# Optimization experiments

Hardware: AMD Instinct MI355X
Metric: run time of the kernel (lower is better)

Reference implementation:

```python
import jax, jax.numpy as jnp
import numpy as np

N_NODES = 100000
N_EDGES = 1600000
D_IN = 128
HIDDEN = 128
N_CLASS = 10
N_LAYERS = 3


def setup_inputs() -> dict:
    key = jax.random.key(0)
    ks = jax.random.split(key, 12)
    x = jax.random.normal(ks[0], (N_NODES, D_IN), dtype=jnp.float32)
    edge_index = jax.random.randint(ks[1], (2, N_EDGES), 0, N_NODES, dtype=jnp.int64)
    edge_weight = jax.random.uniform(ks[2], (N_EDGES,), dtype=jnp.float32)
    # Per-layer GIN MLP params. D_IN == HIDDEN so all 3 layers stack cleanly.
    s = 1.0 / np.sqrt(HIDDEN)
    Wa = jax.random.uniform(ks[3], (N_LAYERS, HIDDEN, HIDDEN), minval=-s, maxval=s, dtype=jnp.float32)
    ba = jax.random.uniform(ks[4], (N_LAYERS, HIDDEN), minval=-s, maxval=s, dtype=jnp.float32)
    Wb = jax.random.uniform(ks[5], (N_LAYERS, HIDDEN, HIDDEN), minval=-s, maxval=s, dtype=jnp.float32)
    bb = jax.random.uniform(ks[6], (N_LAYERS, HIDDEN), minval=-s, maxval=s, dtype=jnp.float32)
    fcW = jax.random.uniform(ks[7], (HIDDEN, N_CLASS), minval=-s, maxval=s, dtype=jnp.float32)
    fcb = jax.random.uniform(ks[8], (N_CLASS,), minval=-s, maxval=s, dtype=jnp.float32)
    return {"x": x, "edge_index": edge_index, "edge_weight": edge_weight,
            "Wa": Wa, "ba": ba, "Wb": Wb, "bb": bb, "fcW": fcW, "fcb": fcb}


def reference(x, edge_index, edge_weight, Wa, ba, Wb, bb, fcW, fcb):
    # NOTE: edge_weight is loaded in the original forward but never used
    # (GINConv is invoked with only (x, edge_index)); we faithfully ignore it.
    src = edge_index[0]
    dst = edge_index[1]
    h = x
    for i in range(N_LAYERS):
        # GIN aggregation: (1 + eps) * h + sum_{j in N(i)} h_j, with eps = 0
        agg = jax.ops.segment_sum(h[src], dst, num_segments=N_NODES)  # [N, H]
        z = h + agg
        # 2-layer MLP: Linear -> ELU -> Linear -> ELU
        z = jax.nn.elu(z @ Wa[i] + ba[i])
        h = jax.nn.elu(z @ Wb[i] + bb[i])
    return h @ fcW + fcb  # [N, n_class]
```

## Files before the change

kernel.cpp:

```cpp
#include <hip/hip_runtime.h>
#include <hip/hip_bf16.h>
#include <math.h>

#define N_NODES 100000
#define N_PAD 100032
#define N_EDGES 1600000
#define HID 128
#define N_CLASS 10

#define NR2 256
#define RANGE2 391
#define PCAP2 8192
#define P_BLOCKS 512
#define P_SLICE (N_EDGES / P_BLOCKS)

typedef float f32x4 __attribute__((ext_vector_type(4)));
typedef short short8 __attribute__((ext_vector_type(8)));
typedef unsigned short us4 __attribute__((ext_vector_type(4)));

__device__ __forceinline__ unsigned short f2bf(float x) {
    unsigned u = __float_as_uint(x);
    unsigned r = u + 0x7FFF + ((u >> 16) & 1);
    return (unsigned short)(r >> 16);
}
__device__ __forceinline__ float bf2f(unsigned short h) {
    return __uint_as_float(((unsigned)h) << 16);
}
__device__ __forceinline__ float elu(float x) {
    return x > 0.f ? x : (expf(x) - 1.f);
}


__global__ __launch_bounds__(256) void part_k(const int* __restrict__ src,
                                              const int* __restrict__ dst,
                                              int* __restrict__ gcnt,
                                              unsigned* __restrict__ gbuf) {
    __shared__ unsigned stash[P_SLICE];
    __shared__ unsigned char rbuf[P_SLICE];
    __shared__ int hist[NR2], cur[NR2], base[NR2];
    hist[threadIdx.x] = 0;
    cur[threadIdx.x] = 0;
    __syncthreads();
    const int e0 = blockIdx.x * P_SLICE;
    for (int i = threadIdx.x; i < P_SLICE; i += 256) {
        unsigned s = (unsigned)src[e0 + i];
        unsigned d = (unsigned)dst[e0 + i];
        unsigned r = d / RANGE2;
        unsigned dloc = d - r * RANGE2;
        stash[i] = s | (dloc << 17);
        rbuf[i] = (unsigned char)r;
        atomicAdd(&hist[r], 1);
    }
    __syncthreads();
    base[threadIdx.x] = atomicAdd(&gcnt[threadIdx.x], hist[threadIdx.x]);
    __syncthreads();
    for (int i = threadIdx.x; i < P_SLICE; i += 256) {
        unsigned r = rbuf[i];
        int off = atomicAdd(&cur[r], 1);
        int pos = base[r] + off;
        if (pos < PCAP2) gbuf[(size_t)r * PCAP2 + pos] = stash[i];
    }
}

__global__ void scanc_k(const int* __restrict__ gcnt, int* __restrict__ colbase,
                        int* __restrict__ row_ptr) {
    __shared__ int sh[NR2];
    int v = gcnt[threadIdx.x];
    sh[threadIdx.x] = v;
    __syncthreads();
    for (int off = 1; off < NR2; off <<= 1) {
        int t = (threadIdx.x >= off) ? sh[threadIdx.x - off] : 0;
        __syncthreads();
        sh[threadIdx.x] += t;
        __syncthreads();
    }
    colbase[threadIdx.x] = sh[threadIdx.x] - v;
    if (threadIdx.x == 0) row_ptr[N_NODES] = N_EDGES;
}

__global__ __launch_bounds__(256) void csort_k(const unsigned* __restrict__ gbuf,
                                               const int* __restrict__ gcnt,
                                               const int* __restrict__ colbase,
                                               int* __restrict__ row_ptr,
                                               int* __restrict__ col) {
    __shared__ int sorted[PCAP2];
    __shared__ int hist[512];
    __shared__ int cnt[512];
    __shared__ int run[400];
    const int q = blockIdx.x;
    const int tid = threadIdx.x;
    const int n2 = gcnt[q];
    const int cb = colbase[q];
    const int node0 = q * RANGE2;
    const unsigned* buf = gbuf + (size_t)q * PCAP2;

    hist[tid] = 0; hist[tid + 256] = 0;
    __syncthreads();
    for (int i = tid; i < n2; i += 256)
        atomicAdd(&hist[buf[i] >> 17], 1);
    __syncthreads();
    cnt[tid] = hist[tid];
    cnt[tid + 256] = hist[tid + 256];
    __syncthreads();
    for (int off = 1; off < 512; off <<= 1) {
        int v0 = (tid >= off) ? hist[tid - off] : 0;
        int v1 = hist[tid + 256 - off];
        __syncthreads();
        hist[tid] += v0;
        hist[tid + 256] += v1;
        __syncthreads();
    }
#pragma unroll
    for (int b = 0; b < 2; b++) {
        int i = tid + 256 * b;
        if (i < RANGE2) {
            int excl = hist[i] - cnt[i];
            run[i] = excl;
            int node = node0 + i;
            if (node < N_NODES) row_ptr[node] = cb + excl;
        }
    }
    __syncthreads();
    for (int i = tid; i < n2; i += 256) {
        unsigned w = buf[i];
        int pos = atomicAdd(&run[w >> 17], 1);
        sorted[pos] = (int)(w & 0x1FFFF);
    }
    __syncthreads();
    for (int i = tid; i < n2; i += 256) col[cb + i] = sorted[i];
}

__global__ __launch_bounds__(256) void cast_k(const float* __restrict__ x,
                                              unsigned short* __restrict__ hb) {
    int i = blockIdx.x * blockDim.x + threadIdx.x;
    if (i < N_NODES * (HID / 4)) {
        float4 v = ((const float4*)x)[i];
        us4 o = {f2bf(v.x), f2bf(v.y), f2bf(v.z), f2bf(v.w)};
        ((us4*)hb)[i] = o;
    }
}

__global__ void wsplit_k(const float* __restrict__ Wa, const float* __restrict__ Wb,
                         unsigned short* __restrict__ Whp,
                         unsigned short* __restrict__ Wlp) {
    int f = blockIdx.x * blockDim.x + threadIdx.x;
    if (f >= 6 * 16384) return;
    int g = f >> 14;
    int r = f & 16383;
    int j = r & 7;
    int L = (r >> 3) & 63;
    int t = r >> 9;
    int kb = t >> 3, nt = t & 7;
    int k = kb * 32 + ((L >> 4) & 3) * 8 + j;
    int n = nt * 16 + (L & 15);
    int layer = g >> 1;
    const float* W = (g & 1) ? Wb : Wa;
    float w = W[layer * 16384 + k * 128 + n];
    unsigned short hi = f2bf(w);
    unsigned short lo = f2bf(w - bf2f(hi));
    Whp[f] = hi;
    Wlp[f] = lo;
}

__global__ void fcsplit_k(const float* __restrict__ fcW,
                          unsigned short* __restrict__ fcWph,
                          unsigned short* __restrict__ fcWpl) {
    int f = blockIdx.x * blockDim.x + threadIdx.x;
    if (f >= 2048) return;
    int j = f & 7;
    int L = (f >> 3) & 63;
    int kb = f >> 9;
    int k = kb * 32 + ((L >> 4) & 3) * 8 + j;
    int n = L & 15;
    float w = (n < N_CLASS) ? fcW[k * N_CLASS + n] : 0.f;
    unsigned short hi = f2bf(w);
    unsigned short lo = f2bf(w - bf2f(hi));
    fcWph[f] = hi;
    fcWpl[f] = lo;
}

__device__ __forceinline__ float4 us4f(us4 v) {
    float4 o;
    o.x = bf2f(v.x); o.y = bf2f(v.y); o.z = bf2f(v.z); o.w = bf2f(v.w);
    return o;
}

__global__ __launch_bounds__(256) void agg_k(const unsigned short* __restrict__ h,
                                             const int* __restrict__ row_ptr,
                                             const int* __restrict__ col,
                                             float* __restrict__ z) {
    const int half = (blockIdx.x * blockDim.x + threadIdx.x) >> 5;
    const int lane = threadIdx.x & 31;
    const int halfbase = threadIdx.x & 32;
    if (half >= N_NODES) return;
    const us4* hp = (const us4*)h;
    float4 acc = us4f(hp[(size_t)half * 32 + lane]);
    const int beg = row_ptr[half];
    const int end = row_ptr[half + 1];

    for (int base = beg; base < end; base += 32) {
        const int n = min(32, end - base);
        int myidx = (lane < n) ? col[base + lane] : 0;
        int j = 0;
        for (; j + 4 <= n; j += 4) {
            int i0 = __shfl(myidx, halfbase + j + 0, 64);
            int i1 = __shfl(myidx, halfbase + j + 1, 64);
            int i2 = __shfl(myidx, halfbase + j + 2, 64);
            int i3 = __shfl(myidx, halfbase + j + 3, 64);
            float4 v0 = us4f(hp[(size_t)i0 * 32 + lane]);
            float4 v1 = us4f(hp[(size_t)i1 * 32 + lane]);
            float4 v2 = us4f(hp[(size_t)i2 * 32 + lane]);
            float4 v3 = us4f(hp[(size_t)i3 * 32 + lane]);
            acc.x += v0.x; acc.y += v0.y; acc.z += v0.z; acc.w += v0.w;
            acc.x += v1.x; acc.y += v1.y; acc.z += v1.z; acc.w += v1.w;
            acc.x += v2.x; acc.y += v2.y; acc.z += v2.z; acc.w += v2.w;
            acc.x += v3.x; acc.y += v3.y; acc.z += v3.z; acc.w += v3.w;
        }
        for (; j < n; j++) {
            int i0 = __shfl(myidx, halfbase + j, 64);
            float4 v0 = us4f(hp[(size_t)i0 * 32 + lane]);
            acc.x += v0.x; acc.y += v0.y; acc.z += v0.z; acc.w += v0.w;
        }
    }
    ((float4*)z)[(size_t)half * 32 + lane] = acc;
}

__device__ __forceinline__ void gemm_phase(
    const unsigned short* Aph_, const unsigned short* Apl_,
    const unsigned short* __restrict__ Whi_g,
    const unsigned short* __restrict__ Wlo_g,
    const float* __restrict__ bias, int tid, f32x4 acc[2][4]) {
    const int L = tid & 63;
    const int w = tid >> 6;
    const int mt0 = (w >> 1) * 2;
    const int nt0 = (w & 1) * 4;
    const int lan15 = L & 15;
#pragma unroll
    for (int n = 0; n < 4; n++) {
        float b = bias[(nt0 + n) * 16 + lan15];
        f32x4 bv = {b, b, b, b};
        acc[0][n] = bv;
        acc[1][n] = bv;
    }
#pragma unroll
    for (int kb = 0; kb < 4; kb++) {
        short8 ah0 = *(const short8*)&Aph_[(((mt0 + 0) * 4 + kb) * 64 + L) * 8];
        short8 ah1 = *(const short8*)&Aph_[(((mt0 + 1) * 4 + kb) * 64 + L) * 8];
        short8 al0 = *(const short8*)&Apl_[(((mt0 + 0) * 4 + kb) * 64 + L) * 8];
        short8 al1 = *(const short8*)&Apl_[(((mt0 + 1) * 4 + kb) * 64 + L) * 8];
#pragma unroll
        for (int n = 0; n < 4; n++) {
            int widx = ((kb * 8 + nt0 + n) * 64 + L) * 8;
            short8 bh = *(const short8*)&Whi_g[widx];
            short8 bl = *(const short8*)&Wlo_g[widx];
            acc[0][n] = __builtin_amdgcn_mfma_f32_16x16x32_bf16(ah0, bh, acc[0][n], 0, 0, 0);
            acc[1][n] = __builtin_amdgcn_mfma_f32_16x16x32_bf16(ah1, bh, acc[1][n], 0, 0, 0);
            acc[0][n] = __builtin_amdgcn_mfma_f32_16x16x32_bf16(al0, bh, acc[0][n], 0, 0, 0);
            acc[1][n] = __builtin_amdgcn_mfma_f32_16x16x32_bf16(al1, bh, acc[1][n], 0, 0, 0);
            acc[0][n] = __builtin_amdgcn_mfma_f32_16x16x32_bf16(ah0, bl, acc[0][n], 0, 0, 0);
            acc[1][n] = __builtin_amdgcn_mfma_f32_16x16x32_bf16(ah1, bl, acc[1][n], 0, 0, 0);
        }
    }
}

template <int FC>
__device__ __forceinline__ void mlp_body(
    const float* __restrict__ zin,
    const unsigned short* __restrict__ Wahp, const unsigned short* __restrict__ Walp,
    const unsigned short* __restrict__ Wbhp, const unsigned short* __restrict__ Wblp,
    const float* __restrict__ ba, const float* __restrict__ bb,
    unsigned short* __restrict__ hout,
    const unsigned short* __restrict__ fcWph, const unsigned short* __restrict__ fcWpl,
    const float* __restrict__ fcb, float* __restrict__ out) {
    __shared__ unsigned short Aph[8192];
    __shared__ unsigned short Apl[8192];

    const int tid = threadIdx.x;
    const int L = tid & 63;
    const int w = tid >> 6;
    const int mt0 = (w >> 1) * 2;
    const int nt0 = (w & 1) * 4;
    const int lan15 = L & 15;
    const int quad = L >> 4;
    const size_t node_base = (size_t)blockIdx.x * 64;

    {
        const float4* zin4 = (const float4*)(zin + node_base * HID);
#pragma unroll
        for (int r = 0; r < 8; r++) {
            int f = tid + 256 * r;
            int m = f >> 5;
            int k0 = (f & 31) * 4;
            float4 zv = zin4[f];
            int kb = k0 >> 5;
            int q = (k0 & 31) >> 3;
            int j0 = k0 & 7;
            int idx = (((m >> 4) * 4 + kb) * 64 + ((m & 15) + 16 * q)) * 8 + j0;
            unsigned short hx = f2bf(zv.x), hy = f2bf(zv.y),
                           hz = f2bf(zv.z), hw = f2bf(zv.w);
            us4 h4 = {hx, hy, hz, hw};
            us4 l4 = {f2bf(zv.x - bf2f(hx)), f2bf(zv.y - bf2f(hy)),
                      f2bf(zv.z - bf2f(hz)), f2bf(zv.w - bf2f(hw))};
            *(us4*)&Aph[idx] = h4;
            *(us4*)&Apl[idx] = l4;
        }
    }
    __syncthreads();

    {
        f32x4 acc[2][4];
        gemm_phase(Aph, Apl, Wahp, Walp, ba, tid, acc);
        __syncthreads();
#pragma unroll
        for (int i = 0; i < 2; i++) {
#pragma unroll
            for (int n = 0; n < 4; n++) {
                int kdim = (nt0 + n) * 16 + lan15;
                int kb2 = kdim >> 5;
                int q2 = (kdim & 31) >> 3;
                int j2 = kdim & 7;
#pragma unroll
                for (int r = 0; r < 4; r++) {
                    float v = elu(acc[i][n][r]);
                    int mrow = quad * 4 + r;
                    unsigned short hi = f2bf(v);
                    unsigned short lo = f2bf(v - bf2f(hi));
                    int idx = (((mt0 + i) * 4 + kb2) * 64 + (mrow + 16 * q2)) * 8 + j2;
                    Aph[idx] = hi;
                    Apl[idx] = lo;
                }
            }
        }
    }
    __syncthreads();

    {
        f32x4 acc[2][4];
        gemm_phase(Aph, Apl, Wbhp, Wblp, bb, tid, acc);
        if (FC == 0) {
#pragma unroll
            for (int i = 0; i < 2; i++) {
#pragma unroll
                for (int n = 0; n < 4; n++) {
                    int ncol = (nt0 + n) * 16 + lan15;
#pragma unroll
                    for (int r = 0; r < 4; r++) {
                        int mrow = (mt0 + i) * 16 + quad * 4 + r;
                        hout[(node_base + mrow) * HID + ncol] = f2bf(elu(acc[i][n][r]));
                    }
                }
            }
        } else {
            __syncthreads();
#pragma unroll
            for (int i = 0; i < 2; i++) {
#pragma unroll
                for (int n = 0; n < 4; n++) {
                    int kdim = (nt0 + n) * 16 + lan15;
                    int kb2 = kdim >> 5;
                    int q2 = (kdim & 31) >> 3;
                    int j2 = kdim & 7;
#pragma unroll
                    for (int r = 0; r < 4; r++) {
                        float v = elu(acc[i][n][r]);
                        int mrow = quad * 4 + r;
                        int idx = (((mt0 + i) * 4 + kb2) * 64 + (mrow + 16 * q2)) * 8 + j2;
                        Aph[idx] = f2bf(v);
                    }
                }
            }
            __syncthreads();
            if ((w & 1) == 0) {
#pragma unroll
                for (int i = 0; i < 2; i++) {
                    int mt = mt0 + i;
                    float b = (lan15 < N_CLASS) ? fcb[lan15] : 0.f;
                    f32x4 acc2 = {b, b, b, b};
#pragma unroll
                    for (int kb = 0; kb < 4; kb++) {
                        short8 a = *(const short8*)&Aph[((mt * 4 + kb) * 64 + L) * 8];
                        short8 bh = *(const short8*)&fcWph[(kb * 64 + L) * 8];
                        short8 bl = *(const short8*)&fcWpl[(kb * 64 + L) * 8];
                        acc2 = __builtin_amdgcn_mfma_f32_16x16x32_bf16(a, bh, acc2, 0, 0, 0);
                        acc2 = __builtin_amdgcn_mfma_f32_16x16x32_bf16(a, bl, acc2, 0, 0, 0);
                    }
#pragma unroll
                    for (int r = 0; r < 4; r++) {
                        size_t node = node_base + mt * 16 + quad * 4 + r;
                        if (node < N_NODES && lan15 < N_CLASS)
                            out[node * N_CLASS + lan15] = acc2[r];
                    }
                }
            }
        }
    }
}

__global__ __launch_bounds__(256) void mlp2_k(
    const float* __restrict__ zin,
    const unsigned short* __restrict__ Wahp, const unsigned short* __restrict__ Walp,
    const unsigned short* __restrict__ Wbhp, const unsigned short* __restrict__ Wblp,
    const float* __restrict__ ba, const float* __restrict__ bb,
    unsigned short* __restrict__ hout) {
    mlp_body<0>(zin, Wahp, Walp, Wbhp, Wblp, ba, bb, hout,
                nullptr, nullptr, nullptr, nullptr);
}

__global__ __launch_bounds__(256) void mlp3_k(
    const float* __restrict__ zin,
    const unsigned short* __restrict__ Wahp, const unsigned short* __restrict__ Walp,
    const unsigned short* __restrict__ Wbhp, const unsigned short* __restrict__ Wblp,
    const float* __restrict__ ba, const float* __restrict__ bb,
    const unsigned short* __restrict__ fcWph, const unsigned short* __restrict__ fcWpl,
    const float* __restrict__ fcb, float* __restrict__ out) {
    mlp_body<1>(zin, Wahp, Walp, Wbhp, Wblp, ba, bb, nullptr,
                fcWph, fcWpl, fcb, out);
}


extern "C" void kernel_launch(void* const* d_in, const int* in_sizes, int n_in,
                              void* d_out, int out_size, void* d_ws, size_t ws_size,
                              hipStream_t stream) {
    const float* x = (const float*)d_in[0];
    const int* ei = (const int*)d_in[1];
    const float* Wa = (const float*)d_in[3];
    const float* ba = (const float*)d_in[4];
    const float* Wb = (const float*)d_in[5];
    const float* bb = (const float*)d_in[6];
    const float* fcW = (const float*)d_in[7];
    const float* fcb = (const float*)d_in[8];
    float* out = (float*)d_out;

    const int* src = ei;
    const int* dst = ei + N_EDGES;

    char* w = (char*)d_ws;
    float* zbuf = (float*)w;          w += (size_t)N_PAD * HID * 4;
    unsigned short* hb = (unsigned short*)w; w += (size_t)N_PAD * HID * 2;
    int* row_ptr = (int*)w;  w += ((size_t)N_NODES + 8) * 4;
    int* gcnt = (int*)w;     w += NR2 * 4;
    int* colbase = (int*)w;  w += NR2 * 4;
    int* col = (int*)w;      w += (size_t)N_EDGES * 4;
    unsigned short* Whp = (unsigned short*)w; w += 6 * 16384 * 2;
    unsigned short* Wlp = (unsigned short*)w; w += 6 * 16384 * 2;
    unsigned short* fcWph = (unsigned short*)w; w += 2048 * 2;
    unsigned short* fcWpl = (unsigned short*)w; w += 2048 * 2;
    unsigned* gbuf = (unsigned*)w; w += (size_t)NR2 * PCAP2 * 4;

    wsplit_k<<<(6 * 16384 + 255) / 256, 256, 0, stream>>>(Wa, Wb, Whp, Wlp);
    fcsplit_k<<<8, 256, 0, stream>>>(fcW, fcWph, fcWpl);
    cast_k<<<(N_NODES * (HID / 4) + 255) / 256, 256, 0, stream>>>(x, hb);

    hipMemsetAsync(gcnt, 0, NR2 * 4, stream);
    part_k<<<P_BLOCKS, 256, 0, stream>>>(src, dst, gcnt, gbuf);
    scanc_k<<<1, 256, 0, stream>>>(gcnt, colbase, row_ptr);
    csort_k<<<NR2, 256, 0, stream>>>(gbuf, gcnt, colbase, row_ptr, col);

    const int AGG_BLOCKS = (N_NODES * 32 + 255) / 256;
    const int MLP_BLOCKS = (N_NODES + 63) / 64;

    agg_k<<<AGG_BLOCKS, 256, 0, stream>>>(hb, row_ptr, col, zbuf);
    mlp2_k<<<MLP_BLOCKS, 256, 0, stream>>>(zbuf, Whp, Wlp, Whp + 16384, Wlp + 16384,
                                           ba, bb, hb);
    agg_k<<<AGG_BLOCKS, 256, 0, stream>>>(hb, row_ptr, col, zbuf);
    mlp2_k<<<MLP_BLOCKS, 256, 0, stream>>>(zbuf, Whp + 2 * 16384, Wlp + 2 * 16384,
                                           Whp + 3 * 16384, Wlp + 3 * 16384,
                                           ba + 128, bb + 128, hb);
    agg_k<<<AGG_BLOCKS, 256, 0, stream>>>(hb, row_ptr, col, zbuf);
    mlp3_k<<<MLP_BLOCKS, 256, 0, stream>>>(zbuf, Whp + 4 * 16384, Wlp + 4 * 16384,
                                           Whp + 5 * 16384, Wlp + 5 * 16384,
                                           ba + 256, bb + 256,
                                           fcWph, fcWpl, fcb, out);
}
```

Measured before the change: 455.2 us.

## Fuse neighbor aggregation into MLP layer kernels with ping-pong bf16 buffers

Folds the gather-sum aggregation into the per-layer MLP kernel: each 64-node block has its half-waves aggregate 8 nodes each and write the split hi/lo bf16 tiles straight into shared memory. This removes the fp32 z buffer round trip through HBM and three kernel launches per forward. Two bf16 h buffers now alternate between layers so that reads and writes do not overlap. The cost is that the irregular gather now shares a block with the MFMA work and its register and LDS budget, and each block processes its 8 nodes per half-wave serially, which may reduce latency hiding for the gathers.

```diff
diff --git a/kernel.cpp b/kernel.cpp
--- a/kernel.cpp
+++ b/kernel.cpp
@@ -28,6 +28,11 @@
 }
 __device__ __forceinline__ float elu(float x) {
     return x > 0.f ? x : (expf(x) - 1.f);
+}
+__device__ __forceinline__ float4 us4f(us4 v) {
+    float4 o;
+    o.x = bf2f(v.x); o.y = bf2f(v.y); o.z = bf2f(v.z); o.w = bf2f(v.w);
+    return o;
 }
 
 
@@ -179,52 +184,6 @@
     fcWpl[f] = lo;
 }
 
-__device__ __forceinline__ float4 us4f(us4 v) {
-    float4 o;
-    o.x = bf2f(v.x); o.y = bf2f(v.y); o.z = bf2f(v.z); o.w = bf2f(v.w);
-    return o;
-}
-
-__global__ __launch_bounds__(256) void agg_k(const unsigned short* __restrict__ h,
-                                             const int* __restrict__ row_ptr,
-                                             const int* __restrict__ col,
-                                             float* __restrict__ z) {
-    const int half = (blockIdx.x * blockDim.x + threadIdx.x) >> 5;
-    const int lane = threadIdx.x & 31;
-    const int halfbase = threadIdx.x & 32;
-    if (half >= N_NODES) return;
-    const us4* hp = (const us4*)h;
-    float4 acc = us4f(hp[(size_t)half * 32 + lane]);
-    const int beg = row_ptr[half];
-    const int end = row_ptr[half + 1];
-
-    for (int base = beg; base < end; base += 32) {
-        const int n = min(32, end - base);
-        int myidx = (lane < n) ? col[base + lane] : 0;
-        int j = 0;
-        for (; j + 4 <= n; j += 4) {
-            int i0 = __shfl(myidx, halfbase + j + 0, 64);
-            int i1 = __shfl(myidx, halfbase + j + 1, 64);
-            int i2 = __shfl(myidx, halfbase + j + 2, 64);
-            int i3 = __shfl(myidx, halfbase + j + 3, 64);
-            float4 v0 = us4f(hp[(size_t)i0 * 32 + lane]);
-            float4 v1 = us4f(hp[(size_t)i1 * 32 + lane]);
-            float4 v2 = us4f(hp[(size_t)i2 * 32 + lane]);
-            float4 v3 = us4f(hp[(size_t)i3 * 32 + lane]);
-            acc.x += v0.x; acc.y += v0.y; acc.z += v0.z; acc.w += v0.w;
-            acc.x += v1.x; acc.y += v1.y; acc.z += v1.z; acc.w += v1.w;
-            acc.x += v2.x; acc.y += v2.y; acc.z += v2.z; acc.w += v2.w;
-            acc.x += v3.x; acc.y += v3.y; acc.z += v3.z; acc.w += v3.w;
-        }
-        for (; j < n; j++) {
-            int i0 = __shfl(myidx, halfbase + j, 64);
-            float4 v0 = us4f(hp[(size_t)i0 * 32 + lane]);
-            acc.x += v0.x; acc.y += v0.y; acc.z += v0.z; acc.w += v0.w;
-        }
-    }
-    ((float4*)z)[(size_t)half * 32 + lane] = acc;
-}
-
 __device__ __forceinline__ void gemm_phase(
     const unsigned short* Aph_, const unsigned short* Apl_,
     const unsigned short* __restrict__ Whi_g,
@@ -264,8 +223,9 @@
 }
 
 template <int FC>
-__device__ __forceinline__ void mlp_body(
-    const float* __restrict__ zin,
+__device__ __forceinline__ void layer_body(
+    const unsigned short* __restrict__ hin,
+    const int* __restrict__ row_ptr, const int* __restrict__ col,
     const unsigned short* __restrict__ Wahp, const unsigned short* __restrict__ Walp,
     const unsigned short* __restrict__ Wbhp, const unsigned short* __restrict__ Wblp,
     const float* __restrict__ ba, const float* __restrict__ bb,
@@ -285,22 +245,54 @@
     const size_t node_base = (size_t)blockIdx.x * 64;
 
     {
-        const float4* zin4 = (const float4*)(zin + node_base * HID);
-#pragma unroll
-        for (int r = 0; r < 8; r++) {
-            int f = tid + 256 * r;
-            int m = f >> 5;
-            int k0 = (f & 31) * 4;
-            float4 zv = zin4[f];
-            int kb = k0 >> 5;
-            int q = (k0 & 31) >> 3;
-            int j0 = k0 & 7;
-            int idx = (((m >> 4) * 4 + kb) * 64 + ((m & 15) + 16 * q)) * 8 + j0;
-            unsigned short hx = f2bf(zv.x), hy = f2bf(zv.y),
-                           hz = f2bf(zv.z), hw = f2bf(zv.w);
-            us4 h4 = {hx, hy, hz, hw};
-            us4 l4 = {f2bf(zv.x - bf2f(hx)), f2bf(zv.y - bf2f(hy)),
-                      f2bf(zv.z - bf2f(hz)), f2bf(zv.w - bf2f(hw))};
+        const int hwv = tid >> 5;
+        const int lane = tid & 31;
+        const int halfbase = tid & 32;
+        const us4* hp = (const us4*)hin;
+        const int k0 = lane * 4;
+        const int kb = k0 >> 5;
+        const int q = (k0 & 31) >> 3;
+        const int j0 = k0 & 7;
+#pragma unroll 1
+        for (int i = 0; i < 8; i++) {
+            const int m = hwv * 8 + i;
+            const int node = (int)node_base + m;
+            float4 acc = {0.f, 0.f, 0.f, 0.f};
+            if (node < N_NODES) {
+                acc = us4f(hp[(size_t)node * 32 + lane]);
+                const int beg = row_ptr[node];
+                const int end = row_ptr[node + 1];
+                for (int base = beg; base < end; base += 32) {
+                    const int n = min(32, end - base);
+                    int myidx = (lane < n) ? col[base + lane] : 0;
+                    int j = 0;
+                    for (; j + 4 <= n; j += 4) {
+                        int i0 = __shfl(myidx, halfbase + j + 0, 64);
+                        int i1 = __shfl(myidx, halfbase + j + 1, 64);
+                        int i2 = __shfl(myidx, halfbase + j + 2, 64);
+                        int i3 = __shfl(myidx, halfbase + j + 3, 64);
+                        float4 v0 = us4f(hp[(size_t)i0 * 32 + lane]);
+                        float4 v1 = us4f(hp[(size_t)i1 * 32 + lane]);
+                        float4 v2 = us4f(hp[(size_t)i2 * 32 + lane]);
+                        float4 v3 = us4f(hp[(size_t)i3 * 32 + lane]);
+                        acc.x += v0.x; acc.y += v0.y; acc.z += v0.z; acc.w += v0.w;
+                        acc.x += v1.x; acc.y += v1.y; acc.z += v1.z; acc.w += v1.w;
+                        acc.x += v2.x; acc.y += v2.y; acc.z += v2.z; acc.w += v2.w;
+                        acc.x += v3.x; acc.y += v3.y; acc.z += v3.z; acc.w += v3.w;
+                    }
+                    for (; j < n; j++) {
+                        int i0 = __shfl(myidx, halfbase + j, 64);
+                        float4 v0 = us4f(hp[(size_t)i0 * 32 + lane]);
+                        acc.x += v0.x; acc.y += v0.y; acc.z += v0.z; acc.w += v0.w;
+                    }
+                }
+            }
+            const int idx = (((m >> 4) * 4 + kb) * 64 + ((m & 15) + 16 * q)) * 8 + j0;
+            unsigned short sx = f2bf(acc.x), sy = f2bf(acc.y),
+                           sz = f2bf(acc.z), sw = f2bf(acc.w);
+            us4 h4 = {sx, sy, sz, sw};
+            us4 l4 = {f2bf(acc.x - bf2f(sx)), f2bf(acc.y - bf2f(sy)),
+                      f2bf(acc.z - bf2f(sz)), f2bf(acc.w - bf2f(sw))};
             *(us4*)&Aph[idx] = h4;
             *(us4*)&Apl[idx] = l4;
         }
@@ -396,25 +388,27 @@
     }
 }
 
-__global__ __launch_bounds__(256) void mlp2_k(
-    const float* __restrict__ zin,
+__global__ __launch_bounds__(256) void layer_mid_k(
+    const unsigned short* __restrict__ hin,
+    const int* __restrict__ row_ptr, const int* __restrict__ col,
     const unsigned short* __restrict__ Wahp, const unsigned short* __restrict__ Walp,
     const unsigned short* __restrict__ Wbhp, const unsigned short* __restrict__ Wblp,
     const float* __restrict__ ba, const float* __restrict__ bb,
     unsigned short* __restrict__ hout) {
-    mlp_body<0>(zin, Wahp, Walp, Wbhp, Wblp, ba, bb, hout,
-                nullptr, nullptr, nullptr, nullptr);
-}
-
-__global__ __launch_bounds__(256) void mlp3_k(
-    const float* __restrict__ zin,
+    layer_body<0>(hin, row_ptr, col, Wahp, Walp, Wbhp, Wblp, ba, bb, hout,
+                  nullptr, nullptr, nullptr, nullptr);
+}
+
+__global__ __launch_bounds__(256) void layer_fc_k(
+    const unsigned short* __restrict__ hin,
+    const int* __restrict__ row_ptr, const int* __restrict__ col,
     const unsigned short* __restrict__ Wahp, const unsigned short* __restrict__ Walp,
     const unsigned short* __restrict__ Wbhp, const unsigned short* __restrict__ Wblp,
     const float* __restrict__ ba, const float* __restrict__ bb,
     const unsigned short* __restrict__ fcWph, const unsigned short* __restrict__ fcWpl,
     const float* __restrict__ fcb, float* __restrict__ out) {
-    mlp_body<1>(zin, Wahp, Walp, Wbhp, Wblp, ba, bb, nullptr,
-                fcWph, fcWpl, fcb, out);
+    layer_body<1>(hin, row_ptr, col, Wahp, Walp, Wbhp, Wblp, ba, bb, nullptr,
+                  fcWph, fcWpl, fcb, out);
 }
 
 
@@ -435,8 +429,8 @@
     const int* dst = ei + N_EDGES;
 
     char* w = (char*)d_ws;
-    float* zbuf = (float*)w;          w += (size_t)N_PAD * HID * 4;
-    unsigned short* hb = (unsigned short*)w; w += (size_t)N_PAD * HID * 2;
+    unsigned short* hbA = (unsigned short*)w; w += (size_t)N_PAD * HID * 2;
+    unsigned short* hbB = (unsigned short*)w; w += (size_t)N_PAD * HID * 2;
     int* row_ptr = (int*)w;  w += ((size_t)N_NODES + 8) * 4;
     int* gcnt = (int*)w;     w += NR2 * 4;
     int* colbase = (int*)w;  w += NR2 * 4;
@@ -449,26 +443,25 @@
 
     wsplit_k<<<(6 * 16384 + 255) / 256, 256, 0, stream>>>(Wa, Wb, Whp, Wlp);
     fcsplit_k<<<8, 256, 0, stream>>>(fcW, fcWph, fcWpl);
-    cast_k<<<(N_NODES * (HID / 4) + 255) / 256, 256, 0, stream>>>(x, hb);
+    cast_k<<<(N_NODES * (HID / 4) + 255) / 256, 256, 0, stream>>>(x, hbA);
 
     hipMemsetAsync(gcnt, 0, NR2 * 4, stream);
     part_k<<<P_BLOCKS, 256, 0, stream>>>(src, dst, gcnt, gbuf);
     scanc_k<<<1, 256, 0, stream>>>(gcnt, colbase, row_ptr);
     csort_k<<<NR2, 256, 0, stream>>>(gbuf, gcnt, colbase, row_ptr, col);
 
-    const int AGG_BLOCKS = (N_NODES * 32 + 255) / 256;
-    const int MLP_BLOCKS = (N_NODES + 63) / 64;
-
-    agg_k<<<AGG_BLOCKS, 256, 0, stream>>>(hb, row_ptr, col, zbuf);
-    mlp2_k<<<MLP_BLOCKS, 256, 0, stream>>>(zbuf, Whp, Wlp, Whp + 16384, Wlp + 16384,
-                                           ba, bb, hb);
-    agg_k<<<AGG_BLOCKS, 256, 0, stream>>>(hb, row_ptr, col, zbuf);
-    mlp2_k<<<MLP_BLOCKS, 256, 0, stream>>>(zbuf, Whp + 2 * 16384, Wlp + 2 * 16384,
-                                           Whp + 3 * 16384, Wlp + 3 * 16384,
-                                           ba + 128, bb + 128, hb);
-    agg_k<<<AGG_BLOCKS, 256, 0, stream>>>(hb, row_ptr, col, zbuf);
-    mlp3_k<<<MLP_BLOCKS, 256, 0, stream>>>(zbuf, Whp + 4 * 16384, Wlp + 4 * 16384,
-                                           Whp + 5 * 16384, Wlp + 5 * 16384,
-                                           ba + 256, bb + 256,
-                                           fcWph, fcWpl, fcb, out);
-}
+    const int LAYER_BLOCKS = (N_NODES + 63) / 64;
+
+    layer_mid_k<<<LAYER_BLOCKS, 256, 0, stream>>>(hbA, row_ptr, col,
+                                                  Whp, Wlp, Whp + 16384, Wlp + 16384,
+                                                  ba, bb, hbB);
+    layer_mid_k<<<LAYER_BLOCKS, 256, 0, stream>>>(hbB, row_ptr, col,
+                                                  Whp + 2 * 16384, Wlp + 2 * 16384,
+                                                  Whp + 3 * 16384, Wlp + 3 * 16384,
+                                                  ba + 128, bb + 128, hbA);
+    layer_fc_k<<<LAYER_BLOCKS, 256, 0, stream>>>(hbA, row_ptr, col,
+                                                 Whp + 4 * 16384, Wlp + 4 * 16384,
+                                                 Whp + 5 * 16384, Wlp + 5 * 16384,
+                                                 ba + 256, bb + 256,
+                                                 fcWph, fcWpl, fcb, out);
+}
```

Measured after the change: 471.7 us. +3.6%, slower.
